# Optimization experiments

Measured on AMD Instinct MI355X. Metric: run time of the kernel, lower is better.

## Reference

```python
import jax, jax.numpy as jnp
import numpy as np

T, H, W_, CIN, LAT, HID, OUT, NHL = 32, 64, 64, 3, 256, 256, 3, 3
OMEGA = 30.0  # SIREN sine frequency


def _uniform(key, shape, fan_in):
    b = np.sqrt(6.0 / fan_in) / OMEGA
    return jax.random.uniform(key, shape, jnp.float32, -b, b)


def setup_inputs() -> dict:
    key = jax.random.key(0)
    ks = jax.random.split(key, 10)
    return {
        "coords": jax.random.normal(ks[0], (T, H, W_, CIN), jnp.float32),
        "latents": jax.random.normal(ks[1], (T, LAT), jnp.float32),
        # shared SIREN weights (nf_net): W stored as (out, in) like nn.Linear
        "W0": _uniform(ks[2], (HID, CIN), CIN),
        "b0": jnp.zeros((HID,), jnp.float32),
        "Wh": _uniform(ks[3], (NHL, HID, HID), HID),
        "bh": jnp.zeros((NHL, HID), jnp.float32),
        "Wf": _uniform(ks[4], (OUT, HID), HID),
        "bf": jnp.zeros((OUT,), jnp.float32),
        # hypernet weight generators (hw_net), no bias
        "HW0": _uniform(ks[5], (HID * CIN, LAT), LAT),
        "HWh": _uniform(ks[6], (NHL, HID * HID, LAT), LAT),
        # hypernet bias generators (hb_net), no bias
        "HB": _uniform(ks[7], (NHL + 1, HID, LAT), LAT),
    }


def reference(coords, latents, W0, b0, Wh, bh, Wf, bf, HW0, HWh, HB):
    t = latents.shape[0]
    # per-frame hyper biases for all layers: (t, NHL+1, HID)
    hb = jnp.einsum('tl,khl->tkh', latents, HB)
    # layer 0: per-frame weight (t, HID, CIN)
    hw0 = (latents @ HW0.T).reshape(t, HID, CIN)
    x = coords  # (t,h,w,CIN)
    x = (x @ W0.T + b0
         + jnp.einsum('thwi,toi->thwo', x, hw0)
         + hb[:, 0][:, None, None, :])
    x = jnp.sin(OMEGA * x)
    for i in range(NHL):
        hw = (latents @ HWh[i].T).reshape(t, HID, HID)  # (t, HID, HID)
        x = (x @ Wh[i].T + bh[i]
             + jnp.einsum('thwi,toi->thwo', x, hw)
             + hb[:, i + 1][:, None, None, :])
        x = jnp.sin(OMEGA * x)
    return x @ Wf.T + bf  # (t,h,w,OUT)
```

## Files before the change

kernel.cpp:

```cpp
#include <hip/hip_runtime.h>
#include <cstdint>
#include <cstddef>

typedef __attribute__((ext_vector_type(8))) _Float16 f16x8;
typedef __attribute__((ext_vector_type(16))) float f32x16;

#define LO_SCALE 2048.0f
#define LO_INV   (1.0f / 2048.0f)

union H8 { f16x8 v; _Float16 h[8]; };

__global__ __launch_bounds__(256) void kab(
    const float* __restrict__ latents, const float* __restrict__ W0,
    const float* __restrict__ b0, const float* __restrict__ bh,
    const float* __restrict__ HW0, const float* __restrict__ HB,
    const float* __restrict__ Wh, const float* __restrict__ HWh,
    _Float16* __restrict__ w0blob, float* __restrict__ beff,
    _Float16* __restrict__ whblob) {
  __shared__ float lat_t[8192];
  int tid = threadIdx.x, bid = blockIdx.x;

  if (bid >= 768) {
    int id = (bid - 768) * 256 + tid;
    if (id < 32768) {
      int t = id >> 10, rem = id & 1023;
      int r2 = rem & 127, part = r2 >> 6, lane = r2 & 63;
      int nf = rem >> 7;
      int o = nf * 32 + (lane & 31), kc = lane >> 5;
      const float* lat = latents + t * 256;
      H8 outv;
#pragma unroll
      for (int j = 0; j < 8; ++j) outv.h[j] = (_Float16)0.0f;
#pragma unroll
      for (int j = 0; j < 8; ++j) {
        int i = kc * 8 + j;
        if (i < 3) {
          const float* row = HW0 + (o * 3 + i) * 256;
          float s = W0[o * 3 + i];
          for (int k = 0; k < 256; k += 4)
            s += row[k] * lat[k] + row[k + 1] * lat[k + 1] +
                 row[k + 2] * lat[k + 2] + row[k + 3] * lat[k + 3];
          _Float16 hi = (_Float16)s;
          outv.h[j] = part ? (_Float16)((s - (float)hi) * LO_SCALE) : hi;
        }
      }
      *(f16x8*)(w0blob + (size_t)id * 8) = outv.v;
    } else {
      int v = id - 32768;
      int t = v >> 10, k = (v >> 8) & 3, hm = v & 255;
      float base = (k == 0) ? b0[hm] : bh[(k - 1) * 256 + hm];
      const float* lat = latents + t * 256;
      const float* row = HB + (size_t)(k * 256 + hm) * 256;
      float s = base;
      for (int kk = 0; kk < 256; kk += 4)
        s += row[kk] * lat[kk] + row[kk + 1] * lat[kk + 1] +
             row[kk + 2] * lat[kk + 2] + row[kk + 3] * lat[kk + 3];
      beff[v] = s;
    }
    return;
  }

  int h = bid & 1, ks = (bid >> 1) & 15, nf = (bid >> 5) & 7, l = bid >> 8;

  {
    int f = tid >> 3, kb = (tid & 7) * 32;
#pragma unroll
    for (int m = 0; m < 32; m += 4) {
      float4 v = *(const float4*)(latents + f * 256 + kb + m);
      lat_t[(kb + m + 0) * 32 + f] = v.x;
      lat_t[(kb + m + 1) * 32 + f] = v.y;
      lat_t[(kb + m + 2) * 32 + f] = v.z;
      lat_t[(kb + m + 3) * 32 + f] = v.w;
    }
  }
  __syncthreads();

  int oo = tid >> 3, jj = tid & 7;
  int o = nf * 32 + oo;
  int i = ks * 16 + h * 8 + jj;
  int r = o * 256 + i;
  const float* rowp = HWh + ((size_t)l * 65536 + (size_t)r) * 256;

  float acc[32];
#pragma unroll
  for (int f = 0; f < 32; ++f) acc[f] = 0.f;

  float curf[16], nxtf[16];
#pragma unroll
  for (int q = 0; q < 4; ++q)
    *(float4*)(curf + q * 4) = *(const float4*)(rowp + q * 4);

  for (int kc = 0; kc < 16; ++kc) {
    if (kc < 15) {
#pragma unroll
      for (int q = 0; q < 4; ++q)
        *(float4*)(nxtf + q * 4) = *(const float4*)(rowp + (kc + 1) * 16 + q * 4);
    }
    const float* lp = lat_t + kc * 512;
#pragma unroll
    for (int m = 0; m < 16; ++m) {
      float hw = curf[m];
#pragma unroll
      for (int fq = 0; fq < 8; ++fq) {
        float4 lv = *(const float4*)(lp + m * 32 + fq * 4);
        acc[fq * 4 + 0] += hw * lv.x;
        acc[fq * 4 + 1] += hw * lv.y;
        acc[fq * 4 + 2] += hw * lv.z;
        acc[fq * 4 + 3] += hw * lv.w;
      }
    }
#pragma unroll
    for (int q = 0; q < 16; ++q) curf[q] = nxtf[q];
  }

  float whv = Wh[l * 65536 + r];
  size_t cbase = (size_t)(nf * 16 + ks) * 1024 + (size_t)h * 256 + (size_t)tid;
#pragma unroll
  for (int t = 0; t < 32; ++t) {
    float w = acc[t] + whv;
    _Float16 hi = (_Float16)w;
    _Float16 lo = (_Float16)((w - (float)hi) * LO_SCALE);
    size_t b = (size_t)(t * 3 + l) * 131072 + cbase;
    whblob[b] = hi;
    whblob[b + 512] = lo;
  }
}

__global__ __launch_bounds__(512, 2) void kb_siren(
    const float* __restrict__ coords, const _Float16* __restrict__ whblob,
    const _Float16* __restrict__ w0blob, const float* __restrict__ beff,
    const float* __restrict__ Wf, const float* __restrict__ bf,
    float* __restrict__ out) {
  __shared__ _Float16 xs_hi[128 * 264];
  __shared__ _Float16 xs_lo[128 * 264];
  __shared__ float wf_s[768];
  __shared__ float red[1536];
  int tid = threadIdx.x;
  int bid0 = blockIdx.x;
  int bid = (bid0 & 7) * 128 + (bid0 >> 3);
  int t = bid >> 5, tile = bid & 31;
  int wv = tid >> 6, lane = tid & 63, col = lane & 31, h = lane >> 5;

  if (tid < 192) *(float4*)(wf_s + tid * 4) = *(const float4*)(Wf + tid * 4);
  if (tid < 128) {
    const float* cp = coords + (size_t)(t * 4096 + tile * 128 + tid) * 3;
    float c0 = cp[0], c1 = cp[1], c2 = cp[2];
    H8 hv, lv, z;
#pragma unroll
    for (int j = 0; j < 8; ++j) { hv.h[j] = (_Float16)0.f; lv.h[j] = (_Float16)0.f; z.h[j] = (_Float16)0.f; }
    _Float16 h0 = (_Float16)c0, h1 = (_Float16)c1, h2 = (_Float16)c2;
    hv.h[0] = h0; hv.h[1] = h1; hv.h[2] = h2;
    lv.h[0] = (_Float16)((c0 - (float)h0) * LO_SCALE);
    lv.h[1] = (_Float16)((c1 - (float)h1) * LO_SCALE);
    lv.h[2] = (_Float16)((c2 - (float)h2) * LO_SCALE);
    *(f16x8*)(xs_hi + tid * 264) = hv.v;
    *(f16x8*)(xs_lo + tid * 264) = lv.v;
    *(f16x8*)(xs_hi + tid * 264 + 8) = z.v;
    *(f16x8*)(xs_lo + tid * 264 + 8) = z.v;
  }
  __syncthreads();

  f32x16 accA[4], accB[4];

  auto init_bias = [&](int bk) {
    const float* bp = beff + ((t * 4 + bk) << 8) + wv * 32 + h * 4;
#pragma unroll
    for (int rq = 0; rq < 4; ++rq) {
      float4 bvv = *(const float4*)(bp + rq * 8);
      float ba[4];
      *(float4*)ba = bvv;
#pragma unroll
      for (int q = 0; q < 4; ++q) {
#pragma unroll
        for (int pf = 0; pf < 4; ++pf) {
          accA[pf][rq * 4 + q] = ba[q];
          accB[pf][rq * 4 + q] = 0.f;
        }
      }
    }
  };

  auto aptr = [&](const _Float16* blobL, int NS, int ks) {
    return blobL + (size_t)((wv * NS + ks) * 2) * 512 + lane * 8;
  };

  auto mfma_ks = [&](f16x8 a0, f16x8 a1, int ks) {
#pragma unroll
    for (int pf = 0; pf < 4; ++pf) {
      int off = (pf * 32 + col) * 264 + ks * 16 + h * 8;
      f16x8 bh_ = *(const f16x8*)(xs_hi + off);
      f16x8 bl_ = *(const f16x8*)(xs_lo + off);
      accA[pf] = __builtin_amdgcn_mfma_f32_32x32x16_f16(a0, bh_, accA[pf], 0, 0, 0);
      accB[pf] = __builtin_amdgcn_mfma_f32_32x32x16_f16(a0, bl_, accB[pf], 0, 0, 0);
      accB[pf] = __builtin_amdgcn_mfma_f32_32x32x16_f16(a1, bh_, accB[pf], 0, 0, 0);
    }
  };

  auto epilogue = [&]() {
#pragma unroll
    for (int pf = 0; pf < 4; ++pf)
#pragma unroll
      for (int r = 0; r < 16; ++r)
        accA[pf][r] = __sinf(30.0f * (accA[pf][r] + accB[pf][r] * LO_INV));
    __syncthreads();
#pragma unroll
    for (int pf = 0; pf < 4; ++pf)
#pragma unroll
      for (int g = 0; g < 2; ++g) {
        float seq[8];
#pragma unroll
        for (int q = 0; q < 4; ++q) {
          float oa = accA[pf][8 * g + q];
          float ob = accA[pf][8 * g + 4 + q];
          float send = h ? oa : ob;
          float recv = __shfl_xor(send, 32, 64);
          seq[q]     = h ? recv : oa;
          seq[4 + q] = h ? ob : recv;
        }
        H8 hv, lv;
#pragma unroll
        for (int j = 0; j < 8; ++j) {
          _Float16 hi = (_Float16)seq[j];
          hv.h[j] = hi;
          lv.h[j] = (_Float16)((seq[j] - (float)hi) * LO_SCALE);
        }
        int off = (pf * 32 + col) * 264 + wv * 32 + g * 16 + h * 8;
        *(f16x8*)(xs_hi + off) = hv.v;
        *(f16x8*)(xs_lo + off) = lv.v;
      }
    __syncthreads();
  };

  const _Float16* bl0 = whblob + (size_t)(t * 3) * 131072;

  init_bias(0);
  {
    const _Float16* p = aptr(w0blob + (size_t)t * 8192, 1, 0);
    f16x8 a0 = *(const f16x8*)p, a1 = *(const f16x8*)(p + 512);
    mfma_ks(a0, a1, 0);
  }
  f16x8 c0, c1;
  {
    const _Float16* p = aptr(bl0, 16, 0);
    c0 = *(const f16x8*)p;
    c1 = *(const f16x8*)(p + 512);
  }
  epilogue();

#pragma unroll
  for (int li = 0; li < 3; ++li) {
    init_bias(li + 1);
    const _Float16* bl = whblob + (size_t)(t * 3 + li) * 131072;
    const _Float16* bln = whblob + (size_t)(t * 3 + li + 1) * 131072;
#pragma unroll
    for (int ks = 0; ks < 16; ++ks) {
      f16x8 n0, n1;
      bool have_next = (ks < 15) || (li < 2);
      if (ks < 15) {
        const _Float16* p = aptr(bl, 16, ks + 1);
        n0 = *(const f16x8*)p;
        n1 = *(const f16x8*)(p + 512);
      } else if (li < 2) {
        const _Float16* p = aptr(bln, 16, 0);
        n0 = *(const f16x8*)p;
        n1 = *(const f16x8*)(p + 512);
      }
      mfma_ks(c0, c1, ks);
      if (have_next) { c0 = n0; c1 = n1; }
    }
    epilogue();
  }

  {
    float pc0 = 0.f, pc1 = 0.f, pc2 = 0.f;
    int px = tid & 127, kq = tid >> 7;
#pragma unroll
    for (int cc = 0; cc < 8; ++cc) {
      int k0 = kq * 64 + cc * 8;
      H8 hv, lv;
      hv.v = *(const f16x8*)(xs_hi + px * 264 + k0);
      lv.v = *(const f16x8*)(xs_lo + px * 264 + k0);
#pragma unroll
      for (int j = 0; j < 8; ++j) {
        float xv = (float)hv.h[j] + (float)lv.h[j] * LO_INV;
        pc0 += xv * wf_s[k0 + j];
        pc1 += xv * wf_s[256 + k0 + j];
        pc2 += xv * wf_s[512 + k0 + j];
      }
    }
    red[kq * 384 + px * 3 + 0] = pc0;
    red[kq * 384 + px * 3 + 1] = pc1;
    red[kq * 384 + px * 3 + 2] = pc2;
    __syncthreads();
    if (tid < 384) {
      int p2 = tid / 3, c = tid - p2 * 3;
      float s = bf[c];
#pragma unroll
      for (int q = 0; q < 4; ++q) s += red[q * 384 + p2 * 3 + c];
      out[(size_t)(t * 4096 + tile * 128 + p2) * 3 + c] = s;
    }
  }
}

extern "C" void kernel_launch(void* const* d_in, const int* in_sizes, int n_in,
                              void* d_out, int out_size, void* d_ws, size_t ws_size,
                              hipStream_t stream) {
  const float* coords  = (const float*)d_in[0];
  const float* latents = (const float*)d_in[1];
  const float* W0      = (const float*)d_in[2];
  const float* b0      = (const float*)d_in[3];
  const float* Wh      = (const float*)d_in[4];
  const float* bh      = (const float*)d_in[5];
  const float* Wf      = (const float*)d_in[6];
  const float* bf      = (const float*)d_in[7];
  const float* HW0     = (const float*)d_in[8];
  const float* HWh     = (const float*)d_in[9];
  const float* HB      = (const float*)d_in[10];
  float* outp = (float*)d_out;

  char* w = (char*)d_ws;
  _Float16* whblob = (_Float16*)w;
  _Float16* w0blob = (_Float16*)(w + 25165824);
  float*    beff   = (float*)(w + 25690112);

  kab<<<1024, 256, 0, stream>>>(latents, W0, b0, bh, HW0, HB, Wh, HWh,
                                w0blob, beff, whblob);
  kb_siren<<<1024, 512, 0, stream>>>(coords, whblob, w0blob, beff, Wf, bf, outp);
}
```

Before: 227.1 us.

## Shrink SIREN tile to 64 pixels with 4 output fragments per wave

The SIREN kernel now processes 64-pixel tiles with 256-thread blocks and 2048 blocks instead of 128-pixel tiles with 512 threads. Each wave now owns 4 output-feature fragments against one 32-pixel group, so it reuses each B fragment loaded from LDS across 4 MFMA tiles instead of reusing one A fragment across 4 pixel groups. In exchange, per-frame hyper-weights are read from global memory twice as often, and each wave holds 4x more A registers, which raises register pressure. The sine argument is also folded into a single fma.

```diff
diff --git a/kernel.cpp b/kernel.cpp
--- a/kernel.cpp
+++ b/kernel.cpp
@@ -126,24 +126,25 @@
   }
 }
 
-__global__ __launch_bounds__(512, 2) void kb_siren(
+__global__ __launch_bounds__(256, 2) void kb_siren(
     const float* __restrict__ coords, const _Float16* __restrict__ whblob,
     const _Float16* __restrict__ w0blob, const float* __restrict__ beff,
     const float* __restrict__ Wf, const float* __restrict__ bf,
     float* __restrict__ out) {
-  __shared__ _Float16 xs_hi[128 * 264];
-  __shared__ _Float16 xs_lo[128 * 264];
+  __shared__ _Float16 xs_hi[64 * 264];
+  __shared__ _Float16 xs_lo[64 * 264];
   __shared__ float wf_s[768];
-  __shared__ float red[1536];
+  __shared__ float red[768];
   int tid = threadIdx.x;
   int bid0 = blockIdx.x;
-  int bid = (bid0 & 7) * 128 + (bid0 >> 3);
-  int t = bid >> 5, tile = bid & 31;
+  int bid = (bid0 & 7) * 256 + (bid0 >> 3);
+  int t = bid >> 6, tile = bid & 63;
   int wv = tid >> 6, lane = tid & 63, col = lane & 31, h = lane >> 5;
+  int og = wv >> 1, pg = wv & 1;
 
   if (tid < 192) *(float4*)(wf_s + tid * 4) = *(const float4*)(Wf + tid * 4);
-  if (tid < 128) {
-    const float* cp = coords + (size_t)(t * 4096 + tile * 128 + tid) * 3;
+  if (tid < 64) {
+    const float* cp = coords + (size_t)(t * 4096 + tile * 64 + tid) * 3;
     float c0 = cp[0], c1 = cp[1], c2 = cp[2];
     H8 hv, lv, z;
 #pragma unroll
@@ -163,55 +164,62 @@
   f32x16 accA[4], accB[4];
 
   auto init_bias = [&](int bk) {
-    const float* bp = beff + ((t * 4 + bk) << 8) + wv * 32 + h * 4;
-#pragma unroll
-    for (int rq = 0; rq < 4; ++rq) {
-      float4 bvv = *(const float4*)(bp + rq * 8);
-      float ba[4];
-      *(float4*)ba = bvv;
-#pragma unroll
-      for (int q = 0; q < 4; ++q) {
-#pragma unroll
-        for (int pf = 0; pf < 4; ++pf) {
-          accA[pf][rq * 4 + q] = ba[q];
-          accB[pf][rq * 4 + q] = 0.f;
+#pragma unroll
+    for (int fr = 0; fr < 4; ++fr) {
+      int nf = og * 4 + fr;
+      const float* bp = beff + ((t * 4 + bk) << 8) + nf * 32 + h * 4;
+#pragma unroll
+      for (int rq = 0; rq < 4; ++rq) {
+        float4 bvv = *(const float4*)(bp + rq * 8);
+        float ba[4];
+        *(float4*)ba = bvv;
+#pragma unroll
+        for (int q = 0; q < 4; ++q) {
+          accA[fr][rq * 4 + q] = ba[q];
+          accB[fr][rq * 4 + q] = 0.f;
         }
       }
     }
   };
 
-  auto aptr = [&](const _Float16* blobL, int NS, int ks) {
-    return blobL + (size_t)((wv * NS + ks) * 2) * 512 + lane * 8;
+  auto aload = [&](const _Float16* blobL, int NS, int ks, f16x8 (&a)[4][2]) {
+#pragma unroll
+    for (int fr = 0; fr < 4; ++fr) {
+      int nf = og * 4 + fr;
+      const _Float16* p = blobL + (size_t)((nf * NS + ks) * 2) * 512 + lane * 8;
+      a[fr][0] = *(const f16x8*)p;
+      a[fr][1] = *(const f16x8*)(p + 512);
+    }
   };
 
-  auto mfma_ks = [&](f16x8 a0, f16x8 a1, int ks) {
-#pragma unroll
-    for (int pf = 0; pf < 4; ++pf) {
-      int off = (pf * 32 + col) * 264 + ks * 16 + h * 8;
-      f16x8 bh_ = *(const f16x8*)(xs_hi + off);
-      f16x8 bl_ = *(const f16x8*)(xs_lo + off);
-      accA[pf] = __builtin_amdgcn_mfma_f32_32x32x16_f16(a0, bh_, accA[pf], 0, 0, 0);
-      accB[pf] = __builtin_amdgcn_mfma_f32_32x32x16_f16(a0, bl_, accB[pf], 0, 0, 0);
-      accB[pf] = __builtin_amdgcn_mfma_f32_32x32x16_f16(a1, bh_, accB[pf], 0, 0, 0);
+  auto mfma_ks = [&](f16x8 (&a)[4][2], int ks) {
+    int off = (pg * 32 + col) * 264 + ks * 16 + h * 8;
+    f16x8 bh_ = *(const f16x8*)(xs_hi + off);
+    f16x8 bl_ = *(const f16x8*)(xs_lo + off);
+#pragma unroll
+    for (int fr = 0; fr < 4; ++fr) {
+      accA[fr] = __builtin_amdgcn_mfma_f32_32x32x16_f16(a[fr][0], bh_, accA[fr], 0, 0, 0);
+      accB[fr] = __builtin_amdgcn_mfma_f32_32x32x16_f16(a[fr][0], bl_, accB[fr], 0, 0, 0);
+      accB[fr] = __builtin_amdgcn_mfma_f32_32x32x16_f16(a[fr][1], bh_, accB[fr], 0, 0, 0);
     }
   };
 
   auto epilogue = [&]() {
 #pragma unroll
-    for (int pf = 0; pf < 4; ++pf)
+    for (int fr = 0; fr < 4; ++fr)
 #pragma unroll
       for (int r = 0; r < 16; ++r)
-        accA[pf][r] = __sinf(30.0f * (accA[pf][r] + accB[pf][r] * LO_INV));
+        accA[fr][r] = __sinf(fmaf(accB[fr][r], 30.0f * LO_INV, 30.0f * accA[fr][r]));
     __syncthreads();
 #pragma unroll
-    for (int pf = 0; pf < 4; ++pf)
+    for (int fr = 0; fr < 4; ++fr)
 #pragma unroll
       for (int g = 0; g < 2; ++g) {
         float seq[8];
 #pragma unroll
         for (int q = 0; q < 4; ++q) {
-          float oa = accA[pf][8 * g + q];
-          float ob = accA[pf][8 * g + 4 + q];
+          float oa = accA[fr][8 * g + q];
+          float ob = accA[fr][8 * g + 4 + q];
           float send = h ? oa : ob;
           float recv = __shfl_xor(send, 32, 64);
           seq[q]     = h ? recv : oa;
@@ -224,7 +232,7 @@
           hv.h[j] = hi;
           lv.h[j] = (_Float16)((seq[j] - (float)hi) * LO_SCALE);
         }
-        int off = (pf * 32 + col) * 264 + wv * 32 + g * 16 + h * 8;
+        int off = (pg * 32 + col) * 264 + (og * 4 + fr) * 32 + g * 16 + h * 8;
         *(f16x8*)(xs_hi + off) = hv.v;
         *(f16x8*)(xs_lo + off) = lv.v;
       }
@@ -232,19 +240,12 @@
   };
 
   const _Float16* bl0 = whblob + (size_t)(t * 3) * 131072;
+  f16x8 acur[4][2], anxt[4][2];
 
   init_bias(0);
-  {
-    const _Float16* p = aptr(w0blob + (size_t)t * 8192, 1, 0);
-    f16x8 a0 = *(const f16x8*)p, a1 = *(const f16x8*)(p + 512);
-    mfma_ks(a0, a1, 0);
-  }
-  f16x8 c0, c1;
-  {
-    const _Float16* p = aptr(bl0, 16, 0);
-    c0 = *(const f16x8*)p;
-    c1 = *(const f16x8*)(p + 512);
-  }
+  aload(w0blob + (size_t)t * 8192, 1, 0, acur);
+  mfma_ks(acur, 0);
+  aload(bl0, 16, 0, acur);
   epilogue();
 
 #pragma unroll
@@ -254,26 +255,27 @@
     const _Float16* bln = whblob + (size_t)(t * 3 + li + 1) * 131072;
 #pragma unroll
     for (int ks = 0; ks < 16; ++ks) {
-      f16x8 n0, n1;
       bool have_next = (ks < 15) || (li < 2);
       if (ks < 15) {
-        const _Float16* p = aptr(bl, 16, ks + 1);
-        n0 = *(const f16x8*)p;
-        n1 = *(const f16x8*)(p + 512);
+        aload(bl, 16, ks + 1, anxt);
       } else if (li < 2) {
-        const _Float16* p = aptr(bln, 16, 0);
-        n0 = *(const f16x8*)p;
-        n1 = *(const f16x8*)(p + 512);
-      }
-      mfma_ks(c0, c1, ks);
-      if (have_next) { c0 = n0; c1 = n1; }
+        aload(bln, 16, 0, anxt);
+      }
+      mfma_ks(acur, ks);
+      if (have_next) {
+#pragma unroll
+        for (int fr = 0; fr < 4; ++fr) {
+          acur[fr][0] = anxt[fr][0];
+          acur[fr][1] = anxt[fr][1];
+        }
+      }
     }
     epilogue();
   }
 
   {
     float pc0 = 0.f, pc1 = 0.f, pc2 = 0.f;
-    int px = tid & 127, kq = tid >> 7;
+    int px = tid & 63, kq = tid >> 6;
 #pragma unroll
     for (int cc = 0; cc < 8; ++cc) {
       int k0 = kq * 64 + cc * 8;
@@ -288,16 +290,16 @@
         pc2 += xv * wf_s[512 + k0 + j];
       }
     }
-    red[kq * 384 + px * 3 + 0] = pc0;
-    red[kq * 384 + px * 3 + 1] = pc1;
-    red[kq * 384 + px * 3 + 2] = pc2;
+    red[kq * 192 + px * 3 + 0] = pc0;
+    red[kq * 192 + px * 3 + 1] = pc1;
+    red[kq * 192 + px * 3 + 2] = pc2;
     __syncthreads();
-    if (tid < 384) {
+    if (tid < 192) {
       int p2 = tid / 3, c = tid - p2 * 3;
       float s = bf[c];
 #pragma unroll
-      for (int q = 0; q < 4; ++q) s += red[q * 384 + p2 * 3 + c];
-      out[(size_t)(t * 4096 + tile * 128 + p2) * 3 + c] = s;
+      for (int q = 0; q < 4; ++q) s += red[q * 192 + p2 * 3 + c];
+      out[(size_t)(t * 4096 + tile * 64 + p2) * 3 + c] = s;
     }
   }
 }
@@ -325,5 +327,5 @@
 
   kab<<<1024, 256, 0, stream>>>(latents, W0, b0, bh, HW0, HB, Wh, HWh,
                                 w0blob, beff, whblob);
-  kb_siren<<<1024, 512, 0, stream>>>(coords, whblob, w0blob, beff, Wf, bf, outp);
+  kb_siren<<<2048, 256, 0, stream>>>(coords, whblob, w0blob, beff, Wf, bf, outp);
 }
```

Result: slower. 290.0 us (+27.7%).

## Split pixel tile into two halves and overlap sine epilogue with MFMA

Applied to the files above, without the earlier changes.

Splits each block's 128-pixel tile into two 64-pixel halves with separate accumulators. The sine epilogue of one half is interleaved into the MFMA k-loop of the other half, so transcendental work overlaps with matrix math. The factor OMEGA/(2π) is folded into the generated weights and biases, so the kernel can use v_fract plus v_sin directly. K indices and the Wf layout are permuted so results can be packed into LDS with cvt_pkrtz and no cross-lane shuffles. This trades extra code complexity and register pressure for fewer stalls, and cvt_pkrtz rounds toward zero, which slightly changes the hi/lo split precision.

```diff
diff --git a/kernel.cpp b/kernel.cpp
--- a/kernel.cpp
+++ b/kernel.cpp
@@ -3,12 +3,16 @@
 #include <cstddef>
 
 typedef __attribute__((ext_vector_type(8))) _Float16 f16x8;
+typedef __attribute__((ext_vector_type(2))) __fp16 h2;
 typedef __attribute__((ext_vector_type(16))) float f32x16;
 
 #define LO_SCALE 2048.0f
 #define LO_INV   (1.0f / 2048.0f)
+#define OMEGA_SC 4.774648292756860f
 
 union H8 { f16x8 v; _Float16 h[8]; };
+union HU { f16x8 v; h2 p[4]; };
+
 
 __global__ __launch_bounds__(256) void kab(
     const float* __restrict__ latents, const float* __restrict__ W0,
@@ -33,13 +37,14 @@
       for (int j = 0; j < 8; ++j) outv.h[j] = (_Float16)0.0f;
 #pragma unroll
       for (int j = 0; j < 8; ++j) {
-        int i = kc * 8 + j;
+        int i = (j & 3) + 8 * (j >> 2) + 16 * kc;
         if (i < 3) {
           const float* row = HW0 + (o * 3 + i) * 256;
           float s = W0[o * 3 + i];
           for (int k = 0; k < 256; k += 4)
             s += row[k] * lat[k] + row[k + 1] * lat[k + 1] +
                  row[k + 2] * lat[k + 2] + row[k + 3] * lat[k + 3];
+          s *= OMEGA_SC;
           _Float16 hi = (_Float16)s;
           outv.h[j] = part ? (_Float16)((s - (float)hi) * LO_SCALE) : hi;
         }
@@ -55,7 +60,7 @@
       for (int kk = 0; kk < 256; kk += 4)
         s += row[kk] * lat[kk] + row[kk + 1] * lat[kk + 1] +
              row[kk + 2] * lat[kk + 2] + row[kk + 3] * lat[kk + 3];
-      beff[v] = s;
+      beff[v] = s * OMEGA_SC;
     }
     return;
   }
@@ -77,7 +82,7 @@
 
   int oo = tid >> 3, jj = tid & 7;
   int o = nf * 32 + oo;
-  int i = ks * 16 + h * 8 + jj;
+  int i = (ks >> 1) * 32 + (ks & 1) * 4 + (jj & 3) + 8 * ((jj >> 2) & 1) + 16 * h;
   int r = o * 256 + i;
   const float* rowp = HWh + ((size_t)l * 65536 + (size_t)r) * 256;
 
@@ -117,7 +122,7 @@
   size_t cbase = (size_t)(nf * 16 + ks) * 1024 + (size_t)h * 256 + (size_t)tid;
 #pragma unroll
   for (int t = 0; t < 32; ++t) {
-    float w = acc[t] + whv;
+    float w = (acc[t] + whv) * OMEGA_SC;
     _Float16 hi = (_Float16)w;
     _Float16 lo = (_Float16)((w - (float)hi) * LO_SCALE);
     size_t b = (size_t)(t * 3 + l) * 131072 + cbase;
@@ -131,8 +136,8 @@
     const _Float16* __restrict__ w0blob, const float* __restrict__ beff,
     const float* __restrict__ Wf, const float* __restrict__ bf,
     float* __restrict__ out) {
-  __shared__ _Float16 xs_hi[128 * 264];
-  __shared__ _Float16 xs_lo[128 * 264];
+  __shared__ _Float16 xs_hi[2][64 * 264];
+  __shared__ _Float16 xs_lo[2][64 * 264];
   __shared__ float wf_s[768];
   __shared__ float red[1536];
   int tid = threadIdx.x;
@@ -141,28 +146,35 @@
   int t = bid >> 5, tile = bid & 31;
   int wv = tid >> 6, lane = tid & 63, col = lane & 31, h = lane >> 5;
 
-  if (tid < 192) *(float4*)(wf_s + tid * 4) = *(const float4*)(Wf + tid * 4);
+  if (tid < 192) {
+    int c = tid >> 6;
+    int pq = (tid & 63) * 4;
+    int blk = pq >> 5, p32 = pq & 31, hq = p32 >> 4, rr = p32 & 15;
+    int src = c * 256 + blk * 32 + 8 * (rr >> 2) + 4 * hq;
+    *(float4*)(wf_s + tid * 4) = *(const float4*)(Wf + src);
+  }
   if (tid < 128) {
+    int half = tid >> 6, row = tid & 63;
     const float* cp = coords + (size_t)(t * 4096 + tile * 128 + tid) * 3;
     float c0 = cp[0], c1 = cp[1], c2 = cp[2];
     H8 hv, lv, z;
 #pragma unroll
     for (int j = 0; j < 8; ++j) { hv.h[j] = (_Float16)0.f; lv.h[j] = (_Float16)0.f; z.h[j] = (_Float16)0.f; }
-    _Float16 h0 = (_Float16)c0, h1 = (_Float16)c1, h2 = (_Float16)c2;
-    hv.h[0] = h0; hv.h[1] = h1; hv.h[2] = h2;
+    _Float16 h0 = (_Float16)c0, h1 = (_Float16)c1, h2_ = (_Float16)c2;
+    hv.h[0] = h0; hv.h[1] = h1; hv.h[2] = h2_;
     lv.h[0] = (_Float16)((c0 - (float)h0) * LO_SCALE);
     lv.h[1] = (_Float16)((c1 - (float)h1) * LO_SCALE);
-    lv.h[2] = (_Float16)((c2 - (float)h2) * LO_SCALE);
-    *(f16x8*)(xs_hi + tid * 264) = hv.v;
-    *(f16x8*)(xs_lo + tid * 264) = lv.v;
-    *(f16x8*)(xs_hi + tid * 264 + 8) = z.v;
-    *(f16x8*)(xs_lo + tid * 264 + 8) = z.v;
+    lv.h[2] = (_Float16)((c2 - (float)h2_) * LO_SCALE);
+    *(f16x8*)(xs_hi[half] + row * 264) = hv.v;
+    *(f16x8*)(xs_lo[half] + row * 264) = lv.v;
+    *(f16x8*)(xs_hi[half] + row * 264 + 8) = z.v;
+    *(f16x8*)(xs_lo[half] + row * 264 + 8) = z.v;
   }
   __syncthreads();
 
-  f32x16 accA[4], accB[4];
-
-  auto init_bias = [&](int bk) {
+  f32x16 a0A[2], a0B[2], a1A[2], a1B[2];
+
+  auto init_bias = [&](int bk, f32x16 (&A)[2], f32x16 (&B)[2]) {
     const float* bp = beff + ((t * 4 + bk) << 8) + wv * 32 + h * 4;
 #pragma unroll
     for (int rq = 0; rq < 4; ++rq) {
@@ -171,115 +183,163 @@
       *(float4*)ba = bvv;
 #pragma unroll
       for (int q = 0; q < 4; ++q) {
-#pragma unroll
-        for (int pf = 0; pf < 4; ++pf) {
-          accA[pf][rq * 4 + q] = ba[q];
-          accB[pf][rq * 4 + q] = 0.f;
-        }
-      }
-    }
-  };
-
-  auto aptr = [&](const _Float16* blobL, int NS, int ks) {
-    return blobL + (size_t)((wv * NS + ks) * 2) * 512 + lane * 8;
-  };
-
-  auto mfma_ks = [&](f16x8 a0, f16x8 a1, int ks) {
-#pragma unroll
-    for (int pf = 0; pf < 4; ++pf) {
-      int off = (pf * 32 + col) * 264 + ks * 16 + h * 8;
-      f16x8 bh_ = *(const f16x8*)(xs_hi + off);
-      f16x8 bl_ = *(const f16x8*)(xs_lo + off);
-      accA[pf] = __builtin_amdgcn_mfma_f32_32x32x16_f16(a0, bh_, accA[pf], 0, 0, 0);
-      accB[pf] = __builtin_amdgcn_mfma_f32_32x32x16_f16(a0, bl_, accB[pf], 0, 0, 0);
-      accB[pf] = __builtin_amdgcn_mfma_f32_32x32x16_f16(a1, bh_, accB[pf], 0, 0, 0);
-    }
-  };
-
-  auto epilogue = [&]() {
-#pragma unroll
-    for (int pf = 0; pf < 4; ++pf)
+        A[0][rq * 4 + q] = ba[q];
+        A[1][rq * 4 + q] = ba[q];
+        B[0][rq * 4 + q] = 0.f;
+        B[1][rq * 4 + q] = 0.f;
+      }
+    }
+  };
+
+  auto aload2 = [&](const _Float16* blobL, int NS, int ks, f16x8& ah, f16x8& al) {
+    const _Float16* p = blobL + (size_t)((wv * NS + ks) * 2) * 512 + lane * 8;
+    ah = *(const f16x8*)p;
+    al = *(const f16x8*)(p + 512);
+  };
+
+  auto bload = [&](int half, int ks, f16x8& b0h, f16x8& b0l, f16x8& b1h, f16x8& b1l) {
+    int off0 = col * 264 + ks * 16 + h * 8;
+    int off1 = off0 + 32 * 264;
+    b0h = *(const f16x8*)(xs_hi[half] + off0);
+    b0l = *(const f16x8*)(xs_lo[half] + off0);
+    b1h = *(const f16x8*)(xs_hi[half] + off1);
+    b1l = *(const f16x8*)(xs_lo[half] + off1);
+  };
+
+  auto mfma6 = [&](f16x8 ah, f16x8 al, f16x8 b0h, f16x8 b0l, f16x8 b1h, f16x8 b1l,
+                   f32x16 (&A)[2], f32x16 (&B)[2]) {
+    A[0] = __builtin_amdgcn_mfma_f32_32x32x16_f16(ah, b0h, A[0], 0, 0, 0);
+    A[1] = __builtin_amdgcn_mfma_f32_32x32x16_f16(ah, b1h, A[1], 0, 0, 0);
+    B[0] = __builtin_amdgcn_mfma_f32_32x32x16_f16(ah, b0l, B[0], 0, 0, 0);
+    B[1] = __builtin_amdgcn_mfma_f32_32x32x16_f16(ah, b1l, B[1], 0, 0, 0);
+    B[0] = __builtin_amdgcn_mfma_f32_32x32x16_f16(al, b0h, B[0], 0, 0, 0);
+    B[1] = __builtin_amdgcn_mfma_f32_32x32x16_f16(al, b1h, B[1], 0, 0, 0);
+  };
+
+  auto sin2pi = [](float x) {
+    float f, r;
+    asm("v_fract_f32 %0, %1" : "=v"(f) : "v"(x));
+    asm("v_sin_f32 %0, %1" : "=v"(r) : "v"(f));
+    return r;
+  };
+
+  auto gphase = [&](const _Float16* bl, int half,
+                    f32x16 (&gA)[2], f32x16 (&gB)[2],
+                    f32x16 (&eA)[2], f32x16 (&eB)[2], bool do_epi) {
+    f16x8 cah, cal, cb0h, cb0l, cb1h, cb1l;
+    f16x8 nah, nal, nb0h, nb0l, nb1h, nb1l;
+    aload2(bl, 16, 0, cah, cal);
+    bload(half, 0, cb0h, cb0l, cb1h, cb1l);
+#pragma unroll
+    for (int ks = 0; ks < 16; ++ks) {
+      if (ks < 15) {
+        aload2(bl, 16, ks + 1, nah, nal);
+        bload(half, ks + 1, nb0h, nb0l, nb1h, nb1l);
+      }
+      mfma6(cah, cal, cb0h, cb0l, cb1h, cb1l, gA, gB);
+      if (do_epi) {
+        eA[0][ks] = sin2pi(fmaf(eB[0][ks], LO_INV, eA[0][ks]));
+        eA[1][ks] = sin2pi(fmaf(eB[1][ks], LO_INV, eA[1][ks]));
+      }
+      if (ks < 15) {
+        cah = nah; cal = nal;
+        cb0h = nb0h; cb0l = nb0l; cb1h = nb1h; cb1l = nb1l;
+      }
+    }
+  };
+
+  auto epi_all = [&](f32x16 (&A)[2], f32x16 (&B)[2]) {
+#pragma unroll
+    for (int pf = 0; pf < 2; ++pf)
 #pragma unroll
       for (int r = 0; r < 16; ++r)
-        accA[pf][r] = __sinf(30.0f * (accA[pf][r] + accB[pf][r] * LO_INV));
+        A[pf][r] = sin2pi(fmaf(B[pf][r], LO_INV, A[pf][r]));
+  };
+
+  auto spack = [&](int half, f32x16 (&A)[2], bool lead_bar) {
+    if (lead_bar) __syncthreads();
+#pragma unroll
+    for (int pf = 0; pf < 2; ++pf) {
+      HU h0, h1, l0, l1;
+#pragma unroll
+      for (int q = 0; q < 4; ++q) {
+        float va = A[pf][2 * q], vb = A[pf][2 * q + 1];
+        h2 hp = __builtin_amdgcn_cvt_pkrtz(va, vb);
+        h0.p[q] = hp;
+        l0.p[q] = __builtin_amdgcn_cvt_pkrtz((va - (float)hp[0]) * LO_SCALE,
+                                             (vb - (float)hp[1]) * LO_SCALE);
+        float vc = A[pf][8 + 2 * q], vd = A[pf][8 + 2 * q + 1];
+        h2 hq_ = __builtin_amdgcn_cvt_pkrtz(vc, vd);
+        h1.p[q] = hq_;
+        l1.p[q] = __builtin_amdgcn_cvt_pkrtz((vc - (float)hq_[0]) * LO_SCALE,
+                                             (vd - (float)hq_[1]) * LO_SCALE);
+      }
+      int off = (pf * 32 + col) * 264 + wv * 32 + h * 16;
+      *(f16x8*)(xs_hi[half] + off) = h0.v;
+      *(f16x8*)(xs_hi[half] + off + 8) = h1.v;
+      *(f16x8*)(xs_lo[half] + off) = l0.v;
+      *(f16x8*)(xs_lo[half] + off + 8) = l1.v;
+    }
     __syncthreads();
-#pragma unroll
-    for (int pf = 0; pf < 4; ++pf)
-#pragma unroll
-      for (int g = 0; g < 2; ++g) {
-        float seq[8];
-#pragma unroll
-        for (int q = 0; q < 4; ++q) {
-          float oa = accA[pf][8 * g + q];
-          float ob = accA[pf][8 * g + 4 + q];
-          float send = h ? oa : ob;
-          float recv = __shfl_xor(send, 32, 64);
-          seq[q]     = h ? recv : oa;
-          seq[4 + q] = h ? ob : recv;
-        }
-        H8 hv, lv;
-#pragma unroll
-        for (int j = 0; j < 8; ++j) {
-          _Float16 hi = (_Float16)seq[j];
-          hv.h[j] = hi;
-          lv.h[j] = (_Float16)((seq[j] - (float)hi) * LO_SCALE);
-        }
-        int off = (pf * 32 + col) * 264 + wv * 32 + g * 16 + h * 8;
-        *(f16x8*)(xs_hi + off) = hv.v;
-        *(f16x8*)(xs_lo + off) = lv.v;
-      }
-    __syncthreads();
-  };
-
-  const _Float16* bl0 = whblob + (size_t)(t * 3) * 131072;
-
-  init_bias(0);
+  };
+
+  const _Float16* L0 = whblob + (size_t)(t * 3 + 0) * 131072;
+  const _Float16* L1 = L0 + 131072;
+  const _Float16* L2 = L1 + 131072;
+  const _Float16* W0b = w0blob + (size_t)t * 8192;
+
+  init_bias(0, a0A, a0B);
   {
-    const _Float16* p = aptr(w0blob + (size_t)t * 8192, 1, 0);
-    f16x8 a0 = *(const f16x8*)p, a1 = *(const f16x8*)(p + 512);
-    mfma_ks(a0, a1, 0);
-  }
-  f16x8 c0, c1;
+    f16x8 ah, al, b0h, b0l, b1h, b1l;
+    aload2(W0b, 1, 0, ah, al);
+    bload(0, 0, b0h, b0l, b1h, b1l);
+    mfma6(ah, al, b0h, b0l, b1h, b1l, a0A, a0B);
+  }
+  init_bias(0, a1A, a1B);
   {
-    const _Float16* p = aptr(bl0, 16, 0);
-    c0 = *(const f16x8*)p;
-    c1 = *(const f16x8*)(p + 512);
-  }
-  epilogue();
-
-#pragma unroll
-  for (int li = 0; li < 3; ++li) {
-    init_bias(li + 1);
-    const _Float16* bl = whblob + (size_t)(t * 3 + li) * 131072;
-    const _Float16* bln = whblob + (size_t)(t * 3 + li + 1) * 131072;
-#pragma unroll
-    for (int ks = 0; ks < 16; ++ks) {
-      f16x8 n0, n1;
-      bool have_next = (ks < 15) || (li < 2);
-      if (ks < 15) {
-        const _Float16* p = aptr(bl, 16, ks + 1);
-        n0 = *(const f16x8*)p;
-        n1 = *(const f16x8*)(p + 512);
-      } else if (li < 2) {
-        const _Float16* p = aptr(bln, 16, 0);
-        n0 = *(const f16x8*)p;
-        n1 = *(const f16x8*)(p + 512);
-      }
-      mfma_ks(c0, c1, ks);
-      if (have_next) { c0 = n0; c1 = n1; }
-    }
-    epilogue();
-  }
+    f16x8 ah, al, b0h, b0l, b1h, b1l;
+    aload2(W0b, 1, 0, ah, al);
+    bload(1, 0, b0h, b0l, b1h, b1l);
+    mfma6(ah, al, b0h, b0l, b1h, b1l, a1A, a1B);
+  }
+  epi_all(a0A, a0B);
+  spack(0, a0A, true);
+
+  init_bias(1, a0A, a0B);
+  gphase(L0, 0, a0A, a0B, a1A, a1B, true);
+  spack(1, a1A, false);
+  init_bias(1, a1A, a1B);
+  gphase(L0, 1, a1A, a1B, a0A, a0B, true);
+  spack(0, a0A, false);
+
+  init_bias(2, a0A, a0B);
+  gphase(L1, 0, a0A, a0B, a1A, a1B, true);
+  spack(1, a1A, false);
+  init_bias(2, a1A, a1B);
+  gphase(L1, 1, a1A, a1B, a0A, a0B, true);
+  spack(0, a0A, false);
+
+  init_bias(3, a0A, a0B);
+  gphase(L2, 0, a0A, a0B, a1A, a1B, true);
+  spack(1, a1A, false);
+  init_bias(3, a1A, a1B);
+  gphase(L2, 1, a1A, a1B, a0A, a0B, true);
+  spack(0, a0A, false);
+  epi_all(a1A, a1B);
+  spack(1, a1A, false);
 
   {
     float pc0 = 0.f, pc1 = 0.f, pc2 = 0.f;
     int px = tid & 127, kq = tid >> 7;
+    int half = px >> 6, row = px & 63;
+    const _Float16* xh = xs_hi[half] + row * 264;
+    const _Float16* xl = xs_lo[half] + row * 264;
 #pragma unroll
     for (int cc = 0; cc < 8; ++cc) {
       int k0 = kq * 64 + cc * 8;
       H8 hv, lv;
-      hv.v = *(const f16x8*)(xs_hi + px * 264 + k0);
-      lv.v = *(const f16x8*)(xs_lo + px * 264 + k0);
+      hv.v = *(const f16x8*)(xh + k0);
+      lv.v = *(const f16x8*)(xl + k0);
 #pragma unroll
       for (int j = 0; j < 8; ++j) {
         float xv = (float)hv.h[j] + (float)lv.h[j] * LO_INV;
```

New measurement: 222.7 us. Within noise of the previous version (-2.0%).
